# Optimization experiments

Hardware: AMD Instinct MI355X
Metric: run time of the kernel (lower is better)

Reference implementation:

```python
import jax, jax.numpy as jnp
import numpy as np
from jax import lax


def setup_inputs() -> dict:
    key = jax.random.key(0)
    k1, k2 = jax.random.split(key)
    B, H, W, C = 8, 32, 32, 512
    N = 16384
    feature_batch = jax.random.normal(k1, (B, H, W, C), dtype=jnp.float32)
    mb = jax.random.normal(k2, (N, C), dtype=jnp.float32)
    return {"feature_batch": feature_batch, "mb": mb, "b": 9}


def reference(feature_batch, mb, b):
    B, H, W, C = feature_batch.shape
    fv = feature_batch.reshape(B * H * W, C)                       # (Q, C)
    sq = (
        jnp.sum(fv * fv, axis=1)[:, None]
        + jnp.sum(mb * mb, axis=1)[None, :]
        - 2.0 * (fv @ mb.T)
    )                                                               # (Q, N)
    sq = jnp.maximum(sq, 0.0)  # guard fp round-off before sqrt
    # smallest-b distances, sorted ascending (top_k of negated values)
    neg_topk = lax.top_k(-sq, b)[0]                                 # (Q, b)
    top_k_dists_squared = -neg_topk
    pixel_scores = jnp.sqrt(top_k_dists_squared[:, 0]).reshape(B, H * W)
    max_idx = jnp.argmax(pixel_scores, axis=1)                      # (B,)
    softmax_args = jnp.sqrt(
        top_k_dists_squared.reshape(B, H * W, b)[jnp.arange(B), max_idx, :]
    )                                                               # (B, b)
    image_scores = softmax_args[:, 0]
    if b > 1:
        image_scores = image_scores * (1.0 - jax.nn.softmax(softmax_args, axis=1)[:, 0])
    pixel_scores = pixel_scores.reshape(B, 1, H, W)
    return pixel_scores, image_scores
```

## Files before the change

kernel.cpp:

```cpp
#include <hip/hip_runtime.h>

typedef unsigned short u16;

#define M_ROWS 8192
#define N_ROWS 16384
#define KDIM   512
#define BM     256
#define BN     128
#define BK     32
#define NCHUNKS 16
#define NPER   (N_ROWS / NCHUNKS)
#define TOPK   9

#define ASZ (BM * BK)
#define BSZ (BN * BK)
#define NTT ((NPER / BN) * (KDIM / BK))

typedef __attribute__((ext_vector_type(8)))  short bf16x8;
typedef __attribute__((ext_vector_type(16))) float f32x16;

__device__ __forceinline__ void gload_lds16(const void* g, void* l) {
  __builtin_amdgcn_global_load_lds(
      (const __attribute__((address_space(1))) void*)g,
      (__attribute__((address_space(3))) void*)l,
      16, 0, 0);
}

__device__ __forceinline__ u16 f2bf(float x) {
  union { float f; unsigned u; } c; c.f = x;
  unsigned u = c.u;
  u += 0x7fffu + ((u >> 16) & 1u);
  return (u16)(u >> 16);
}

__device__ __forceinline__ void topk_update(float v, float* best) {
  if (v < best[TOPK - 1]) {
    #pragma unroll
    for (int i = 0; i < TOPK; ++i) {
      float b = best[i];
      best[i] = fminf(b, v);
      v = fmaxf(b, v);
    }
  }
}

__global__ __launch_bounds__(256) void prep_kernel(
    const float* __restrict__ fv, const float* __restrict__ mb,
    u16* __restrict__ fvb, u16* __restrict__ mbb,
    float* __restrict__ nf, float* __restrict__ nm_perm)
{
  int idx = blockIdx.x * 4 + (threadIdx.x >> 6);
  int l = threadIdx.x & 63;
  const float* src; u16* dst;
  if (idx < M_ROWS) {
    src = fv + (size_t)idx * KDIM; dst = fvb + (size_t)idx * KDIM;
  } else {
    int r = idx - M_ROWS;
    src = mb + (size_t)r * KDIM; dst = mbb + (size_t)r * KDIM;
  }
  float4 x0 = ((const float4*)src)[2 * l];
  float4 x1 = ((const float4*)src)[2 * l + 1];
  float s = x0.x * x0.x + x0.y * x0.y + x0.z * x0.z + x0.w * x0.w
          + x1.x * x1.x + x1.y * x1.y + x1.z * x1.z + x1.w * x1.w;
  uint4 o;
  o.x = (unsigned)f2bf(x0.x) | ((unsigned)f2bf(x0.y) << 16);
  o.y = (unsigned)f2bf(x0.z) | ((unsigned)f2bf(x0.w) << 16);
  o.z = (unsigned)f2bf(x1.x) | ((unsigned)f2bf(x1.y) << 16);
  o.w = (unsigned)f2bf(x1.z) | ((unsigned)f2bf(x1.w) << 16);
  ((uint4*)dst)[l] = o;
  #pragma unroll
  for (int off = 32; off > 0; off >>= 1) s += __shfl_down(s, off, 64);
  if (l == 0) {
    if (idx < M_ROWS) {
      nf[idx] = s;
    } else {
      int n  = idx - M_ROWS;
      int ig = n >> 5;
      int w5 = n & 31;
      int h  = (w5 >> 2) & 1;
      int r  = (w5 & 3) | ((w5 >> 3) << 2);
      nm_perm[(ig * 2 + h) * 16 + r] = s;
    }
  }
}

__global__ __launch_bounds__(256, 2) void gemm_topk_kernel(
    const u16* __restrict__ fvb, const u16* __restrict__ mbb,
    const float* __restrict__ nm_perm, float* __restrict__ partial)
{
  extern __shared__ __align__(16) u16 sm[];
  u16* const Asm = sm;
  u16* const Bsm = sm + 3 * ASZ;

  const int t   = threadIdx.x;
  const int l   = t & 63;
  const int w   = t >> 6;
  const int h   = l >> 5;
  const int c31 = l & 31;
  const int xr  = (c31 >> 1) & 3;

  const int m0    = blockIdx.x * BM;
  const int ncoff = blockIdx.y * NPER;

  const int srow = l >> 2;
  const int sc   = ((l & 3) ^ ((l >> 3) & 3)) * 8;

  const u16* aSrc = fvb + (size_t)(m0 + w * 64 + srow) * KDIM + sc;
  const u16* bSrc = mbb + (size_t)(ncoff + w * 32 + srow) * KDIM + sc;

  const int aRd  = (w * 64 + c31) * BK;
  const int ch0  = (h ^ xr) * 8;
  const int ch1  = ch0 ^ 16;

#define STAGE(kc2_, bufS_) do {                                               \
    const size_t ao_ = (size_t)((kc2_) & 15) * BK;                            \
    const size_t so_ = (size_t)((kc2_) >> 4) * ((size_t)BN * KDIM) + ao_;     \
    u16* ad_ = Asm + (bufS_) * ASZ + (w * 64) * BK;                           \
    u16* bd_ = Bsm + (bufS_) * BSZ + (w * 32) * BK;                           \
    gload_lds16(aSrc + ao_,                 ad_);                             \
    gload_lds16(aSrc + ao_ + 16 * KDIM,     ad_ + 16 * BK);                   \
    gload_lds16(aSrc + ao_ + 32 * KDIM,     ad_ + 32 * BK);                   \
    gload_lds16(aSrc + ao_ + 48 * KDIM,     ad_ + 48 * BK);                   \
    gload_lds16(bSrc + so_,                 bd_);                             \
    gload_lds16(bSrc + so_ + 16 * KDIM,     bd_ + 16 * BK);                   \
  } while (0)

  float best[2][TOPK];
  float T[2];
  #pragma unroll
  for (int s = 0; s < 2; ++s) {
    T[s] = 3.4e38f;
    #pragma unroll
    for (int i = 0; i < TOPK; ++i) best[s][i] = 3.4e38f;
  }

  f32x16 acc[2][4];

  STAGE(0, 0);
  STAGE(1, 1);
  asm volatile("s_waitcnt vmcnt(6)" ::: "memory");
  __builtin_amdgcn_s_barrier();

  int bC = 0, bS = 2;
  for (int tt = 0; tt < NTT; ++tt) {
    if ((tt & 15) == 0) {
      #pragma unroll
      for (int s = 0; s < 2; ++s)
        #pragma unroll
        for (int i = 0; i < 4; ++i)
          #pragma unroll
          for (int r = 0; r < 16; ++r) acc[s][i][r] = 0.0f;
    }

    const int kc2 = tt + 2;
    if (kc2 < NTT) STAGE(kc2, bS);

    {
      const u16* Ak = Asm + bC * ASZ;
      const u16* Bk = Bsm + bC * BSZ;
      {
        bf16x8 f0 = *(const bf16x8*)&Ak[aRd + ch0];
        bf16x8 f1 = *(const bf16x8*)&Ak[aRd + 32 * BK + ch0];
        #pragma unroll
        for (int i = 0; i < 4; ++i) {
          bf16x8 mbf = *(const bf16x8*)&Bk[(i * 32 + c31) * BK + ch0];
          acc[0][i] = __builtin_amdgcn_mfma_f32_32x32x16_bf16(mbf, f0, acc[0][i], 0, 0, 0);
          acc[1][i] = __builtin_amdgcn_mfma_f32_32x32x16_bf16(mbf, f1, acc[1][i], 0, 0, 0);
        }
      }
      {
        bf16x8 f0 = *(const bf16x8*)&Ak[aRd + ch1];
        bf16x8 f1 = *(const bf16x8*)&Ak[aRd + 32 * BK + ch1];
        #pragma unroll
        for (int i = 0; i < 4; ++i) {
          bf16x8 mbf = *(const bf16x8*)&Bk[(i * 32 + c31) * BK + ch1];
          acc[0][i] = __builtin_amdgcn_mfma_f32_32x32x16_bf16(mbf, f0, acc[0][i], 0, 0, 0);
          acc[1][i] = __builtin_amdgcn_mfma_f32_32x32x16_bf16(mbf, f1, acc[1][i], 0, 0, 0);
        }
      }
    }

    if (tt < NTT - 1) {
      if (tt < NTT - 2) { asm volatile("s_waitcnt vmcnt(6)" ::: "memory"); }
      else              { asm volatile("s_waitcnt vmcnt(0)" ::: "memory"); }
      __builtin_amdgcn_s_barrier();
    }

    if ((tt & 15) == 15) {
      const int nt    = tt >> 4;
      const int nbase = ncoff + nt * BN;
      #pragma unroll
      for (int i = 0; i < 4; ++i) {
        const float4* np = (const float4*)&nm_perm[(((nbase >> 5) + i) * 2 + h) * 16];
        float4 q0 = np[0], q1 = np[1], q2 = np[2], q3 = np[3];
        #pragma unroll
        for (int s = 0; s < 2; ++s) {
          float v[16];
          v[ 0] = fmaf(-2.0f, acc[s][i][ 0], q0.x);
          v[ 1] = fmaf(-2.0f, acc[s][i][ 1], q0.y);
          v[ 2] = fmaf(-2.0f, acc[s][i][ 2], q0.z);
          v[ 3] = fmaf(-2.0f, acc[s][i][ 3], q0.w);
          v[ 4] = fmaf(-2.0f, acc[s][i][ 4], q1.x);
          v[ 5] = fmaf(-2.0f, acc[s][i][ 5], q1.y);
          v[ 6] = fmaf(-2.0f, acc[s][i][ 6], q1.z);
          v[ 7] = fmaf(-2.0f, acc[s][i][ 7], q1.w);
          v[ 8] = fmaf(-2.0f, acc[s][i][ 8], q2.x);
          v[ 9] = fmaf(-2.0f, acc[s][i][ 9], q2.y);
          v[10] = fmaf(-2.0f, acc[s][i][10], q2.z);
          v[11] = fmaf(-2.0f, acc[s][i][11], q2.w);
          v[12] = fmaf(-2.0f, acc[s][i][12], q3.x);
          v[13] = fmaf(-2.0f, acc[s][i][13], q3.y);
          v[14] = fmaf(-2.0f, acc[s][i][14], q3.z);
          v[15] = fmaf(-2.0f, acc[s][i][15], q3.w);
          float bmin = 3.4e38f;
          #pragma unroll
          for (int r = 0; r < 16; ++r) bmin = fminf(bmin, v[r]);
          if (bmin < T[s]) {
            #pragma unroll
            for (int r = 0; r < 16; ++r) topk_update(v[r], best[s]);
            T[s] = best[s][TOPK - 1];
          }
        }
      }
      #pragma unroll
      for (int s = 0; s < 2; ++s)
        T[s] = fminf(best[s][TOPK - 1], __shfl_xor(best[s][TOPK - 1], 32, 64));
    }

    bC = (bC == 2) ? 0 : bC + 1;
    bS = (bS == 2) ? 0 : bS + 1;
  }

  #pragma unroll
  for (int s = 0; s < 2; ++s) {
    float tmp[TOPK];
    #pragma unroll
    for (int q = 0; q < TOPK; ++q) tmp[q] = __shfl_xor(best[s][q], 32, 64);
    #pragma unroll
    for (int q = 0; q < TOPK; ++q) topk_update(tmp[q], best[s]);
    int m = m0 + w * 64 + s * 32 + c31;
    size_t base = ((size_t)blockIdx.y * M_ROWS + m) * TOPK;
    if (h == 0) {
      #pragma unroll
      for (int q = 0; q < 5; ++q) partial[base + q] = best[s][q];
    } else {
      #pragma unroll
      for (int q = 5; q < TOPK; ++q) partial[base + q] = best[s][q];
    }
  }
}

__global__ __launch_bounds__(256) void merge_kernel(
    const float* __restrict__ partial, const float* __restrict__ nf,
    float* __restrict__ final9, float* __restrict__ out_pix)
{
  int row = blockIdx.x * 256 + threadIdx.x;
  float best[TOPK];
  #pragma unroll
  for (int i = 0; i < TOPK; ++i) best[i] = 3.4e38f;
  for (int s = 0; s < NCHUNKS; ++s) {
    const float* p = &partial[((size_t)s * M_ROWS + row) * TOPK];
    #pragma unroll
    for (int i = 0; i < TOPK; ++i) topk_update(p[i], best);
  }
  float nfr = nf[row];
  float d[TOPK];
  #pragma unroll
  for (int i = 0; i < TOPK; ++i) d[i] = sqrtf(fmaxf(best[i] + nfr, 0.0f));
  out_pix[row] = d[0];
  #pragma unroll
  for (int i = 0; i < TOPK; ++i) final9[(size_t)row * TOPK + i] = d[i];
}

__global__ __launch_bounds__(256) void img_kernel(
    const float* __restrict__ out_pix, const float* __restrict__ final9,
    const int* __restrict__ bptr, float* __restrict__ out_img)
{
  int img = blockIdx.x, t = threadIdx.x;
  float bv = -1.0f; int bi = 0;
  for (int p = t; p < 1024; p += 256) {
    float v = out_pix[img * 1024 + p];
    if (v > bv) { bv = v; bi = p; }
  }
  __shared__ float sv[256];
  __shared__ int   si[256];
  sv[t] = bv; si[t] = bi;
  __syncthreads();
  for (int off = 128; off > 0; off >>= 1) {
    if (t < off) {
      float v2 = sv[t + off]; int i2 = si[t + off];
      if (v2 > sv[t] || (v2 == sv[t] && i2 < si[t])) { sv[t] = v2; si[t] = i2; }
    }
    __syncthreads();
  }
  if (t == 0) {
    int row = img * 1024 + si[0];
    int b = bptr[0];
    float s0 = final9[(size_t)row * TOPK + 0];
    float score = s0;
    if (b > 1) {
      int bb = b < TOPK ? b : TOPK;
      float mx = s0;
      for (int i = 1; i < bb; ++i) mx = fmaxf(mx, final9[(size_t)row * TOPK + i]);
      float den = 0.0f;
      for (int i = 0; i < bb; ++i) den += expf(final9[(size_t)row * TOPK + i] - mx);
      score = s0 * (1.0f - expf(s0 - mx) / den);
    }
    out_img[img] = score;
  }
}

extern "C" void kernel_launch(void* const* d_in, const int* in_sizes, int n_in,
                              void* d_out, int out_size, void* d_ws, size_t ws_size,
                              hipStream_t stream) {
  const float* fv   = (const float*)d_in[0];
  const float* mb   = (const float*)d_in[1];
  const int*   bptr = (const int*)d_in[2];
  float* out = (float*)d_out;

  char* ws = (char*)d_ws;
  u16*   fvb     = (u16*)ws;
  u16*   mbb     = (u16*)(ws + 8388608);
  float* nf      = (float*)(ws + 25165824);
  float* nm_perm = (float*)(ws + 25198592);
  float* partial = (float*)(ws + 25264128);
  float* final9  = (float*)(ws + 29982720);

  hipLaunchKernelGGL(prep_kernel, dim3((M_ROWS + N_ROWS) / 4), dim3(256), 0, stream,
                     fv, mb, fvb, mbb, nf, nm_perm);
  hipLaunchKernelGGL(gemm_topk_kernel, dim3(M_ROWS / BM, NCHUNKS), dim3(256),
                     73728, stream, fvb, mbb, nm_perm, partial);
  hipLaunchKernelGGL(merge_kernel, dim3(M_ROWS / 256), dim3(256), 0, stream,
                     partial, nf, final9, out);
  hipLaunchKernelGGL(img_kernel, dim3(8), dim3(256), 0, stream,
                     out, final9, bptr, out + M_ROWS);
}
```

Before: 312.6 us.

## Halve GEMM M-tile and split warps 2x2 with LDS top-k merge

Shrinks the block tile from 256x128 to 128x128 and arranges the four waves as a 2x2 grid over M and N, so each wave computes a 64x64 sub-tile. The grid grows from 32x16 to 64x16 blocks, shared memory per block drops to 48KB and launch bounds allow three blocks per CU, aiming for more parallelism and occupancy. The two N-halves of each row now hold separate top-k lists, which are combined through shared memory before the partial results are written. The cost is lower operand reuse per block (more global and LDS traffic per FLOP) and an extra synchronized merge step.

```diff
diff --git a/kernel.cpp b/kernel.cpp
--- a/kernel.cpp
+++ b/kernel.cpp
@@ -5,7 +5,7 @@
 #define M_ROWS 8192
 #define N_ROWS 16384
 #define KDIM   512
-#define BM     256
+#define BM     128
 #define BN     128
 #define BK     32
 #define NCHUNKS 16
@@ -84,7 +84,7 @@
   }
 }
 
-__global__ __launch_bounds__(256, 2) void gemm_topk_kernel(
+__global__ __launch_bounds__(256, 3) void gemm_topk_kernel(
     const u16* __restrict__ fvb, const u16* __restrict__ mbb,
     const float* __restrict__ nm_perm, float* __restrict__ partial)
 {
@@ -95,6 +95,8 @@
   const int t   = threadIdx.x;
   const int l   = t & 63;
   const int w   = t >> 6;
+  const int wm  = w >> 1;
+  const int wn  = w & 1;
   const int h   = l >> 5;
   const int c31 = l & 31;
   const int xr  = (c31 >> 1) & 3;
@@ -105,24 +107,25 @@
   const int srow = l >> 2;
   const int sc   = ((l & 3) ^ ((l >> 3) & 3)) * 8;
 
-  const u16* aSrc = fvb + (size_t)(m0 + w * 64 + srow) * KDIM + sc;
+  const u16* aSrc = fvb + (size_t)(m0 + w * 32 + srow) * KDIM + sc;
   const u16* bSrc = mbb + (size_t)(ncoff + w * 32 + srow) * KDIM + sc;
 
-  const int aRd  = (w * 64 + c31) * BK;
+  const int aRd0 = (wm * 64 +      c31) * BK;
+  const int aRd1 = (wm * 64 + 32 + c31) * BK;
+  const int bRd0 = (wn * 64 +      c31) * BK;
+  const int bRd1 = (wn * 64 + 32 + c31) * BK;
   const int ch0  = (h ^ xr) * 8;
   const int ch1  = ch0 ^ 16;
 
 #define STAGE(kc2_, bufS_) do {                                               \
     const size_t ao_ = (size_t)((kc2_) & 15) * BK;                            \
     const size_t so_ = (size_t)((kc2_) >> 4) * ((size_t)BN * KDIM) + ao_;     \
-    u16* ad_ = Asm + (bufS_) * ASZ + (w * 64) * BK;                           \
+    u16* ad_ = Asm + (bufS_) * ASZ + (w * 32) * BK;                           \
     u16* bd_ = Bsm + (bufS_) * BSZ + (w * 32) * BK;                           \
-    gload_lds16(aSrc + ao_,                 ad_);                             \
-    gload_lds16(aSrc + ao_ + 16 * KDIM,     ad_ + 16 * BK);                   \
-    gload_lds16(aSrc + ao_ + 32 * KDIM,     ad_ + 32 * BK);                   \
-    gload_lds16(aSrc + ao_ + 48 * KDIM,     ad_ + 48 * BK);                   \
-    gload_lds16(bSrc + so_,                 bd_);                             \
-    gload_lds16(bSrc + so_ + 16 * KDIM,     bd_ + 16 * BK);                   \
+    gload_lds16(aSrc + ao_,             ad_);                                 \
+    gload_lds16(aSrc + ao_ + 16 * KDIM, ad_ + 16 * BK);                       \
+    gload_lds16(bSrc + so_,             bd_);                                 \
+    gload_lds16(bSrc + so_ + 16 * KDIM, bd_ + 16 * BK);                       \
   } while (0)
 
   float best[2][TOPK];
@@ -134,11 +137,11 @@
     for (int i = 0; i < TOPK; ++i) best[s][i] = 3.4e38f;
   }
 
-  f32x16 acc[2][4];
+  f32x16 acc[2][2];
 
   STAGE(0, 0);
   STAGE(1, 1);
-  asm volatile("s_waitcnt vmcnt(6)" ::: "memory");
+  asm volatile("s_waitcnt vmcnt(4)" ::: "memory");
   __builtin_amdgcn_s_barrier();
 
   int bC = 0, bS = 2;
@@ -147,7 +150,7 @@
       #pragma unroll
       for (int s = 0; s < 2; ++s)
         #pragma unroll
-        for (int i = 0; i < 4; ++i)
+        for (int i = 0; i < 2; ++i)
           #pragma unroll
           for (int r = 0; r < 16; ++r) acc[s][i][r] = 0.0f;
     }
@@ -159,29 +162,29 @@
       const u16* Ak = Asm + bC * ASZ;
       const u16* Bk = Bsm + bC * BSZ;
       {
-        bf16x8 f0 = *(const bf16x8*)&Ak[aRd + ch0];
-        bf16x8 f1 = *(const bf16x8*)&Ak[aRd + 32 * BK + ch0];
-        #pragma unroll
-        for (int i = 0; i < 4; ++i) {
-          bf16x8 mbf = *(const bf16x8*)&Bk[(i * 32 + c31) * BK + ch0];
-          acc[0][i] = __builtin_amdgcn_mfma_f32_32x32x16_bf16(mbf, f0, acc[0][i], 0, 0, 0);
-          acc[1][i] = __builtin_amdgcn_mfma_f32_32x32x16_bf16(mbf, f1, acc[1][i], 0, 0, 0);
-        }
+        bf16x8 f0 = *(const bf16x8*)&Ak[aRd0 + ch0];
+        bf16x8 f1 = *(const bf16x8*)&Ak[aRd1 + ch0];
+        bf16x8 g0 = *(const bf16x8*)&Bk[bRd0 + ch0];
+        bf16x8 g1 = *(const bf16x8*)&Bk[bRd1 + ch0];
+        acc[0][0] = __builtin_amdgcn_mfma_f32_32x32x16_bf16(g0, f0, acc[0][0], 0, 0, 0);
+        acc[0][1] = __builtin_amdgcn_mfma_f32_32x32x16_bf16(g1, f0, acc[0][1], 0, 0, 0);
+        acc[1][0] = __builtin_amdgcn_mfma_f32_32x32x16_bf16(g0, f1, acc[1][0], 0, 0, 0);
+        acc[1][1] = __builtin_amdgcn_mfma_f32_32x32x16_bf16(g1, f1, acc[1][1], 0, 0, 0);
       }
       {
-        bf16x8 f0 = *(const bf16x8*)&Ak[aRd + ch1];
-        bf16x8 f1 = *(const bf16x8*)&Ak[aRd + 32 * BK + ch1];
-        #pragma unroll
-        for (int i = 0; i < 4; ++i) {
-          bf16x8 mbf = *(const bf16x8*)&Bk[(i * 32 + c31) * BK + ch1];
-          acc[0][i] = __builtin_amdgcn_mfma_f32_32x32x16_bf16(mbf, f0, acc[0][i], 0, 0, 0);
-          acc[1][i] = __builtin_amdgcn_mfma_f32_32x32x16_bf16(mbf, f1, acc[1][i], 0, 0, 0);
-        }
+        bf16x8 f0 = *(const bf16x8*)&Ak[aRd0 + ch1];
+        bf16x8 f1 = *(const bf16x8*)&Ak[aRd1 + ch1];
+        bf16x8 g0 = *(const bf16x8*)&Bk[bRd0 + ch1];
+        bf16x8 g1 = *(const bf16x8*)&Bk[bRd1 + ch1];
+        acc[0][0] = __builtin_amdgcn_mfma_f32_32x32x16_bf16(g0, f0, acc[0][0], 0, 0, 0);
+        acc[0][1] = __builtin_amdgcn_mfma_f32_32x32x16_bf16(g1, f0, acc[0][1], 0, 0, 0);
+        acc[1][0] = __builtin_amdgcn_mfma_f32_32x32x16_bf16(g0, f1, acc[1][0], 0, 0, 0);
+        acc[1][1] = __builtin_amdgcn_mfma_f32_32x32x16_bf16(g1, f1, acc[1][1], 0, 0, 0);
       }
     }
 
     if (tt < NTT - 1) {
-      if (tt < NTT - 2) { asm volatile("s_waitcnt vmcnt(6)" ::: "memory"); }
+      if (tt < NTT - 2) { asm volatile("s_waitcnt vmcnt(4)" ::: "memory"); }
       else              { asm volatile("s_waitcnt vmcnt(0)" ::: "memory"); }
       __builtin_amdgcn_s_barrier();
     }
@@ -190,8 +193,9 @@
       const int nt    = tt >> 4;
       const int nbase = ncoff + nt * BN;
       #pragma unroll
-      for (int i = 0; i < 4; ++i) {
-        const float4* np = (const float4*)&nm_perm[(((nbase >> 5) + i) * 2 + h) * 16];
+      for (int i = 0; i < 2; ++i) {
+        const float4* np =
+            (const float4*)&nm_perm[(((nbase >> 5) + wn * 2 + i) * 2 + h) * 16];
         float4 q0 = np[0], q1 = np[1], q2 = np[2], q3 = np[3];
         #pragma unroll
         for (int s = 0; s < 2; ++s) {
@@ -238,14 +242,33 @@
     for (int q = 0; q < TOPK; ++q) tmp[q] = __shfl_xor(best[s][q], 32, 64);
     #pragma unroll
     for (int q = 0; q < TOPK; ++q) topk_update(tmp[q], best[s]);
-    int m = m0 + w * 64 + s * 32 + c31;
-    size_t base = ((size_t)blockIdx.y * M_ROWS + m) * TOPK;
-    if (h == 0) {
-      #pragma unroll
-      for (int q = 0; q < 5; ++q) partial[base + q] = best[s][q];
-    } else {
-      #pragma unroll
-      for (int q = 5; q < TOPK; ++q) partial[base + q] = best[s][q];
+  }
+
+  float* smerge = (float*)sm;
+  __syncthreads();
+  if (wn == 1 && h == 0) {
+    #pragma unroll
+    for (int s = 0; s < 2; ++s)
+      #pragma unroll
+      for (int q = 0; q < TOPK; ++q)
+        smerge[(wm * 64 + s * 32 + c31) * TOPK + q] = best[s][q];
+  }
+  __syncthreads();
+  if (wn == 0) {
+    #pragma unroll
+    for (int s = 0; s < 2; ++s) {
+      const float* p = &smerge[(wm * 64 + s * 32 + c31) * TOPK];
+      #pragma unroll
+      for (int q = 0; q < TOPK; ++q) topk_update(p[q], best[s]);
+      int m = m0 + wm * 64 + s * 32 + c31;
+      size_t base = ((size_t)blockIdx.y * M_ROWS + m) * TOPK;
+      if (h == 0) {
+        #pragma unroll
+        for (int q = 0; q < 5; ++q) partial[base + q] = best[s][q];
+      } else {
+        #pragma unroll
+        for (int q = 5; q < TOPK; ++q) partial[base + q] = best[s][q];
+      }
     }
   }
 }
@@ -329,7 +352,7 @@
   hipLaunchKernelGGL(prep_kernel, dim3((M_ROWS + N_ROWS) / 4), dim3(256), 0, stream,
                      fv, mb, fvb, mbb, nf, nm_perm);
   hipLaunchKernelGGL(gemm_topk_kernel, dim3(M_ROWS / BM, NCHUNKS), dim3(256),
-                     73728, stream, fvb, mbb, nm_perm, partial);
+                     49152, stream, fvb, mbb, nm_perm, partial);
   hipLaunchKernelGGL(merge_kernel, dim3(M_ROWS / 256), dim3(256), 0, stream,
                      partial, nf, final9, out);
   hipLaunchKernelGGL(img_kernel, dim3(8), dim3(256), 0, stream,
```

Result: slower. 348.3 us (+11.4%).

## Fold memory-bank norms into GEMM via extended K and fuse merge with image scoring

Applied to the files above, without the earlier changes.

Extends K from 512 to 544 and packs -||m||^2/2 as a bf16 hi/lo pair against constant 1.0 entries in the query rows, so the MFMA accumulator directly holds x·m - ||m||^2/2. The epilogue then runs a top-k on maxima without loading the permuted norm array or doing per-element FMAs, and scales by -2 only at the final write. The merge and image kernels are fused into one 8-block kernel that recomputes the top-9 for the argmax row, removing the final9 buffer and one launch. The extra K slice adds about 6% more MFMA work and global loads, the merge now runs on only 8 blocks, and the bf16 split of the norm brings a small precision risk.

```diff
diff --git a/kernel.cpp b/kernel.cpp
--- a/kernel.cpp
+++ b/kernel.cpp
@@ -5,6 +5,7 @@
 #define M_ROWS 8192
 #define N_ROWS 16384
 #define KDIM   512
+#define KEXT   544
 #define BM     256
 #define BN     128
 #define BK     32
@@ -14,7 +15,8 @@
 
 #define ASZ (BM * BK)
 #define BSZ (BN * BK)
-#define NTT ((NPER / BN) * (KDIM / BK))
+#define KT  (KEXT / BK)
+#define NTT ((NPER / BN) * KT)
 
 typedef __attribute__((ext_vector_type(8)))  short bf16x8;
 typedef __attribute__((ext_vector_type(16))) float f32x16;
@@ -33,6 +35,11 @@
   return (u16)(u >> 16);
 }
 
+__device__ __forceinline__ float bf2f(u16 x) {
+  union { unsigned u; float f; } c; c.u = ((unsigned)x) << 16;
+  return c.f;
+}
+
 __device__ __forceinline__ void topk_update(float v, float* best) {
   if (v < best[TOPK - 1]) {
     #pragma unroll
@@ -44,19 +51,30 @@
   }
 }
 
+__device__ __forceinline__ void topk_update_max(float v, float* best) {
+  if (v > best[TOPK - 1]) {
+    #pragma unroll
+    for (int i = 0; i < TOPK; ++i) {
+      float b = best[i];
+      best[i] = fmaxf(b, v);
+      v = fminf(b, v);
+    }
+  }
+}
+
 __global__ __launch_bounds__(256) void prep_kernel(
     const float* __restrict__ fv, const float* __restrict__ mb,
-    u16* __restrict__ fvb, u16* __restrict__ mbb,
-    float* __restrict__ nf, float* __restrict__ nm_perm)
+    u16* __restrict__ fvb, u16* __restrict__ mbb, float* __restrict__ nf)
 {
   int idx = blockIdx.x * 4 + (threadIdx.x >> 6);
   int l = threadIdx.x & 63;
   const float* src; u16* dst;
-  if (idx < M_ROWS) {
-    src = fv + (size_t)idx * KDIM; dst = fvb + (size_t)idx * KDIM;
+  const bool isf = idx < M_ROWS;
+  if (isf) {
+    src = fv + (size_t)idx * KDIM; dst = fvb + (size_t)idx * KEXT;
   } else {
     int r = idx - M_ROWS;
-    src = mb + (size_t)r * KDIM; dst = mbb + (size_t)r * KDIM;
+    src = mb + (size_t)r * KDIM; dst = mbb + (size_t)r * KEXT;
   }
   float4 x0 = ((const float4*)src)[2 * l];
   float4 x1 = ((const float4*)src)[2 * l + 1];
@@ -69,24 +87,29 @@
   o.w = (unsigned)f2bf(x1.z) | ((unsigned)f2bf(x1.w) << 16);
   ((uint4*)dst)[l] = o;
   #pragma unroll
-  for (int off = 32; off > 0; off >>= 1) s += __shfl_down(s, off, 64);
-  if (l == 0) {
-    if (idx < M_ROWS) {
-      nf[idx] = s;
-    } else {
-      int n  = idx - M_ROWS;
-      int ig = n >> 5;
-      int w5 = n & 31;
-      int h  = (w5 >> 2) & 1;
-      int r  = (w5 & 3) | ((w5 >> 3) << 2);
-      nm_perm[(ig * 2 + h) * 16 + r] = s;
-    }
-  }
+  for (int off = 32; off > 0; off >>= 1) s += __shfl_xor(s, off, 64);
+  if (l < 4) {
+    uint4 z = {0u, 0u, 0u, 0u};
+    if (l == 0) {
+      unsigned e01;
+      if (isf) {
+        e01 = 0x3F80u | (0x3F80u << 16);
+      } else {
+        float a = 0.5f * s;
+        u16 ah = f2bf(a);
+        u16 al = f2bf(a - bf2f(ah));
+        e01 = (unsigned)(ah ^ 0x8000u) | ((unsigned)(al ^ 0x8000u) << 16);
+      }
+      z.x = e01;
+    }
+    ((uint4*)(dst + KDIM))[l] = z;
+  }
+  if (isf && l == 0) nf[idx] = s;
 }
 
 __global__ __launch_bounds__(256, 2) void gemm_topk_kernel(
     const u16* __restrict__ fvb, const u16* __restrict__ mbb,
-    const float* __restrict__ nm_perm, float* __restrict__ partial)
+    float* __restrict__ partial)
 {
   extern __shared__ __align__(16) u16 sm[];
   u16* const Asm = sm;
@@ -105,45 +128,49 @@
   const int srow = l >> 2;
   const int sc   = ((l & 3) ^ ((l >> 3) & 3)) * 8;
 
-  const u16* aSrc = fvb + (size_t)(m0 + w * 64 + srow) * KDIM + sc;
-  const u16* bSrc = mbb + (size_t)(ncoff + w * 32 + srow) * KDIM + sc;
+  const u16* aSrc = fvb + (size_t)(m0 + w * 64 + srow) * KEXT + sc;
+  const u16* bSrc = mbb + (size_t)(ncoff + w * 32 + srow) * KEXT + sc;
 
   const int aRd  = (w * 64 + c31) * BK;
+  const int bRd  = c31 * BK;
   const int ch0  = (h ^ xr) * 8;
   const int ch1  = ch0 ^ 16;
 
-#define STAGE(kc2_, bufS_) do {                                               \
-    const size_t ao_ = (size_t)((kc2_) & 15) * BK;                            \
-    const size_t so_ = (size_t)((kc2_) >> 4) * ((size_t)BN * KDIM) + ao_;     \
+#define STAGE(koS_, nOffS_, bufS_) do {                                       \
+    const u16* as_ = aSrc + (koS_) * BK;                                      \
+    const u16* bs_ = bSrc + (nOffS_) + (koS_) * BK;                           \
     u16* ad_ = Asm + (bufS_) * ASZ + (w * 64) * BK;                           \
     u16* bd_ = Bsm + (bufS_) * BSZ + (w * 32) * BK;                           \
-    gload_lds16(aSrc + ao_,                 ad_);                             \
-    gload_lds16(aSrc + ao_ + 16 * KDIM,     ad_ + 16 * BK);                   \
-    gload_lds16(aSrc + ao_ + 32 * KDIM,     ad_ + 32 * BK);                   \
-    gload_lds16(aSrc + ao_ + 48 * KDIM,     ad_ + 48 * BK);                   \
-    gload_lds16(bSrc + so_,                 bd_);                             \
-    gload_lds16(bSrc + so_ + 16 * KDIM,     bd_ + 16 * BK);                   \
+    gload_lds16(as_,             ad_);                                        \
+    gload_lds16(as_ + 16 * KEXT, ad_ + 16 * BK);                              \
+    gload_lds16(as_ + 32 * KEXT, ad_ + 32 * BK);                              \
+    gload_lds16(as_ + 48 * KEXT, ad_ + 48 * BK);                              \
+    gload_lds16(bs_,             bd_);                                        \
+    gload_lds16(bs_ + 16 * KEXT, bd_ + 16 * BK);                              \
   } while (0)
 
   float best[2][TOPK];
   float T[2];
   #pragma unroll
   for (int s = 0; s < 2; ++s) {
-    T[s] = 3.4e38f;
-    #pragma unroll
-    for (int i = 0; i < TOPK; ++i) best[s][i] = 3.4e38f;
+    T[s] = -3.4e38f;
+    #pragma unroll
+    for (int i = 0; i < TOPK; ++i) best[s][i] = -3.4e38f;
   }
 
   f32x16 acc[2][4];
 
-  STAGE(0, 0);
-  STAGE(1, 1);
+  STAGE(0, 0, 0);
+  STAGE(1, 0, 1);
   asm volatile("s_waitcnt vmcnt(6)" ::: "memory");
   __builtin_amdgcn_s_barrier();
 
   int bC = 0, bS = 2;
+  int ko = 0;
+  int ko2 = 2;
+  int nOff2 = 0;
   for (int tt = 0; tt < NTT; ++tt) {
-    if ((tt & 15) == 0) {
+    if (ko == 0) {
       #pragma unroll
       for (int s = 0; s < 2; ++s)
         #pragma unroll
@@ -152,28 +179,27 @@
           for (int r = 0; r < 16; ++r) acc[s][i][r] = 0.0f;
     }
 
-    const int kc2 = tt + 2;
-    if (kc2 < NTT) STAGE(kc2, bS);
+    if (tt + 2 < NTT) STAGE(ko2, nOff2, bS);
 
     {
       const u16* Ak = Asm + bC * ASZ;
       const u16* Bk = Bsm + bC * BSZ;
       {
         bf16x8 f0 = *(const bf16x8*)&Ak[aRd + ch0];
-        bf16x8 f1 = *(const bf16x8*)&Ak[aRd + 32 * BK + ch0];
+        bf16x8 f1 = *(const bf16x8*)&Ak[aRd + 1024 + ch0];
         #pragma unroll
         for (int i = 0; i < 4; ++i) {
-          bf16x8 mbf = *(const bf16x8*)&Bk[(i * 32 + c31) * BK + ch0];
+          bf16x8 mbf = *(const bf16x8*)&Bk[bRd + i * 1024 + ch0];
           acc[0][i] = __builtin_amdgcn_mfma_f32_32x32x16_bf16(mbf, f0, acc[0][i], 0, 0, 0);
           acc[1][i] = __builtin_amdgcn_mfma_f32_32x32x16_bf16(mbf, f1, acc[1][i], 0, 0, 0);
         }
       }
       {
         bf16x8 f0 = *(const bf16x8*)&Ak[aRd + ch1];
-        bf16x8 f1 = *(const bf16x8*)&Ak[aRd + 32 * BK + ch1];
+        bf16x8 f1 = *(const bf16x8*)&Ak[aRd + 1024 + ch1];
         #pragma unroll
         for (int i = 0; i < 4; ++i) {
-          bf16x8 mbf = *(const bf16x8*)&Bk[(i * 32 + c31) * BK + ch1];
+          bf16x8 mbf = *(const bf16x8*)&Bk[bRd + i * 1024 + ch1];
           acc[0][i] = __builtin_amdgcn_mfma_f32_32x32x16_bf16(mbf, f0, acc[0][i], 0, 0, 0);
           acc[1][i] = __builtin_amdgcn_mfma_f32_32x32x16_bf16(mbf, f1, acc[1][i], 0, 0, 0);
         }
@@ -186,49 +212,30 @@
       __builtin_amdgcn_s_barrier();
     }
 
-    if ((tt & 15) == 15) {
-      const int nt    = tt >> 4;
-      const int nbase = ncoff + nt * BN;
+    if (ko == 16) {
       #pragma unroll
       for (int i = 0; i < 4; ++i) {
-        const float4* np = (const float4*)&nm_perm[(((nbase >> 5) + i) * 2 + h) * 16];
-        float4 q0 = np[0], q1 = np[1], q2 = np[2], q3 = np[3];
         #pragma unroll
         for (int s = 0; s < 2; ++s) {
-          float v[16];
-          v[ 0] = fmaf(-2.0f, acc[s][i][ 0], q0.x);
-          v[ 1] = fmaf(-2.0f, acc[s][i][ 1], q0.y);
-          v[ 2] = fmaf(-2.0f, acc[s][i][ 2], q0.z);
-          v[ 3] = fmaf(-2.0f, acc[s][i][ 3], q0.w);
-          v[ 4] = fmaf(-2.0f, acc[s][i][ 4], q1.x);
-          v[ 5] = fmaf(-2.0f, acc[s][i][ 5], q1.y);
-          v[ 6] = fmaf(-2.0f, acc[s][i][ 6], q1.z);
-          v[ 7] = fmaf(-2.0f, acc[s][i][ 7], q1.w);
-          v[ 8] = fmaf(-2.0f, acc[s][i][ 8], q2.x);
-          v[ 9] = fmaf(-2.0f, acc[s][i][ 9], q2.y);
-          v[10] = fmaf(-2.0f, acc[s][i][10], q2.z);
-          v[11] = fmaf(-2.0f, acc[s][i][11], q2.w);
-          v[12] = fmaf(-2.0f, acc[s][i][12], q3.x);
-          v[13] = fmaf(-2.0f, acc[s][i][13], q3.y);
-          v[14] = fmaf(-2.0f, acc[s][i][14], q3.z);
-          v[15] = fmaf(-2.0f, acc[s][i][15], q3.w);
-          float bmin = 3.4e38f;
+          float bmax = acc[s][i][0];
           #pragma unroll
-          for (int r = 0; r < 16; ++r) bmin = fminf(bmin, v[r]);
-          if (bmin < T[s]) {
+          for (int r = 1; r < 16; ++r) bmax = fmaxf(bmax, acc[s][i][r]);
+          if (bmax > T[s]) {
             #pragma unroll
-            for (int r = 0; r < 16; ++r) topk_update(v[r], best[s]);
+            for (int r = 0; r < 16; ++r) topk_update_max(acc[s][i][r], best[s]);
             T[s] = best[s][TOPK - 1];
           }
         }
       }
       #pragma unroll
       for (int s = 0; s < 2; ++s)
-        T[s] = fminf(best[s][TOPK - 1], __shfl_xor(best[s][TOPK - 1], 32, 64));
+        T[s] = fmaxf(best[s][TOPK - 1], __shfl_xor(best[s][TOPK - 1], 32, 64));
     }
 
     bC = (bC == 2) ? 0 : bC + 1;
     bS = (bS == 2) ? 0 : bS + 1;
+    ko = (ko == 16) ? 0 : ko + 1;
+    if (ko2 == 16) { ko2 = 0; nOff2 += BN * KEXT; } else { ++ko2; }
   }
 
   #pragma unroll
@@ -237,53 +244,43 @@
     #pragma unroll
     for (int q = 0; q < TOPK; ++q) tmp[q] = __shfl_xor(best[s][q], 32, 64);
     #pragma unroll
-    for (int q = 0; q < TOPK; ++q) topk_update(tmp[q], best[s]);
+    for (int q = 0; q < TOPK; ++q) topk_update_max(tmp[q], best[s]);
     int m = m0 + w * 64 + s * 32 + c31;
     size_t base = ((size_t)blockIdx.y * M_ROWS + m) * TOPK;
     if (h == 0) {
       #pragma unroll
-      for (int q = 0; q < 5; ++q) partial[base + q] = best[s][q];
+      for (int q = 0; q < 5; ++q) partial[base + q] = -2.0f * best[s][q];
     } else {
       #pragma unroll
-      for (int q = 5; q < TOPK; ++q) partial[base + q] = best[s][q];
-    }
-  }
-}
-
-__global__ __launch_bounds__(256) void merge_kernel(
+      for (int q = 5; q < TOPK; ++q) partial[base + q] = -2.0f * best[s][q];
+    }
+  }
+}
+
+__global__ __launch_bounds__(256) void merge_img_kernel(
     const float* __restrict__ partial, const float* __restrict__ nf,
-    float* __restrict__ final9, float* __restrict__ out_pix)
+    const int* __restrict__ bptr, float* __restrict__ out_pix,
+    float* __restrict__ out_img)
 {
-  int row = blockIdx.x * 256 + threadIdx.x;
-  float best[TOPK];
-  #pragma unroll
-  for (int i = 0; i < TOPK; ++i) best[i] = 3.4e38f;
-  for (int s = 0; s < NCHUNKS; ++s) {
-    const float* p = &partial[((size_t)s * M_ROWS + row) * TOPK];
-    #pragma unroll
-    for (int i = 0; i < TOPK; ++i) topk_update(p[i], best);
-  }
-  float nfr = nf[row];
-  float d[TOPK];
-  #pragma unroll
-  for (int i = 0; i < TOPK; ++i) d[i] = sqrtf(fmaxf(best[i] + nfr, 0.0f));
-  out_pix[row] = d[0];
-  #pragma unroll
-  for (int i = 0; i < TOPK; ++i) final9[(size_t)row * TOPK + i] = d[i];
-}
-
-__global__ __launch_bounds__(256) void img_kernel(
-    const float* __restrict__ out_pix, const float* __restrict__ final9,
-    const int* __restrict__ bptr, float* __restrict__ out_img)
-{
-  int img = blockIdx.x, t = threadIdx.x;
-  float bv = -1.0f; int bi = 0;
-  for (int p = t; p < 1024; p += 256) {
-    float v = out_pix[img * 1024 + p];
-    if (v > bv) { bv = v; bi = p; }
-  }
+  const int img = blockIdx.x, t = threadIdx.x;
   __shared__ float sv[256];
   __shared__ int   si[256];
+  float bv = -1.0f; int bi = 0;
+  for (int k = 0; k < 4; ++k) {
+    int p = t + k * 256;
+    int row = img * 1024 + p;
+    float best[TOPK];
+    #pragma unroll
+    for (int i = 0; i < TOPK; ++i) best[i] = 3.4e38f;
+    for (int s = 0; s < NCHUNKS; ++s) {
+      const float* pp = &partial[((size_t)s * M_ROWS + row) * TOPK];
+      #pragma unroll
+      for (int i = 0; i < TOPK; ++i) topk_update(pp[i], best);
+    }
+    float d0 = sqrtf(fmaxf(best[0] + nf[row], 0.0f));
+    out_pix[row] = d0;
+    if (d0 > bv) { bv = d0; bi = p; }
+  }
   sv[t] = bv; si[t] = bi;
   __syncthreads();
   for (int off = 128; off > 0; off >>= 1) {
@@ -295,15 +292,27 @@
   }
   if (t == 0) {
     int row = img * 1024 + si[0];
+    float best[TOPK];
+    #pragma unroll
+    for (int i = 0; i < TOPK; ++i) best[i] = 3.4e38f;
+    for (int s = 0; s < NCHUNKS; ++s) {
+      const float* pp = &partial[((size_t)s * M_ROWS + row) * TOPK];
+      #pragma unroll
+      for (int i = 0; i < TOPK; ++i) topk_update(pp[i], best);
+    }
+    float nfr = nf[row];
+    float d[TOPK];
+    #pragma unroll
+    for (int i = 0; i < TOPK; ++i) d[i] = sqrtf(fmaxf(best[i] + nfr, 0.0f));
     int b = bptr[0];
-    float s0 = final9[(size_t)row * TOPK + 0];
+    float s0 = d[0];
     float score = s0;
     if (b > 1) {
       int bb = b < TOPK ? b : TOPK;
       float mx = s0;
-      for (int i = 1; i < bb; ++i) mx = fmaxf(mx, final9[(size_t)row * TOPK + i]);
+      for (int i = 1; i < bb; ++i) mx = fmaxf(mx, d[i]);
       float den = 0.0f;
-      for (int i = 0; i < bb; ++i) den += expf(final9[(size_t)row * TOPK + i] - mx);
+      for (int i = 0; i < bb; ++i) den += expf(d[i] - mx);
       score = s0 * (1.0f - expf(s0 - mx) / den);
     }
     out_img[img] = score;
@@ -320,18 +329,14 @@
 
   char* ws = (char*)d_ws;
   u16*   fvb     = (u16*)ws;
-  u16*   mbb     = (u16*)(ws + 8388608);
-  float* nf      = (float*)(ws + 25165824);
-  float* nm_perm = (float*)(ws + 25198592);
-  float* partial = (float*)(ws + 25264128);
-  float* final9  = (float*)(ws + 29982720);
+  u16*   mbb     = (u16*)(ws + 8912896);
+  float* nf      = (float*)(ws + 26738688);
+  float* partial = (float*)(ws + 26771456);
 
   hipLaunchKernelGGL(prep_kernel, dim3((M_ROWS + N_ROWS) / 4), dim3(256), 0, stream,
-                     fv, mb, fvb, mbb, nf, nm_perm);
+                     fv, mb, fvb, mbb, nf);
   hipLaunchKernelGGL(gemm_topk_kernel, dim3(M_ROWS / BM, NCHUNKS), dim3(256),
-                     73728, stream, fvb, mbb, nm_perm, partial);
-  hipLaunchKernelGGL(merge_kernel, dim3(M_ROWS / 256), dim3(256), 0, stream,
-                     partial, nf, final9, out);
-  hipLaunchKernelGGL(img_kernel, dim3(8), dim3(256), 0, stream,
-                     out, final9, bptr, out + M_ROWS);
-}
+                     73728, stream, fvb, mbb, partial);
+  hipLaunchKernelGGL(merge_img_kernel, dim3(8), dim3(256), 0, stream,
+                     partial, nf, bptr, out, out + M_ROWS);
+}
```

Measured after the change: 397.1 us. 1.27x slower.

## Widen GEMM tile to 256x256 with 8 waves and in-LDS top-k merge

Applied to the files above, without the earlier changes.

Doubles the N tile (BN 128->256) and the block to 512 threads arranged as a 4x2 wave grid, so each block reuses its A tile across twice as many memory-bank columns. Each wave now stages only 2 A and 2 B rows per k-step, and the waitcnt values are adjusted to match. The two N-half waves holding the same rows merge their top-9 lists through LDS before writing partial results. This costs more LDS per block (96KB), which may limit occupancy, and adds an extra merge step with barriers.

```diff
diff --git a/kernel.cpp b/kernel.cpp
--- a/kernel.cpp
+++ b/kernel.cpp
@@ -6,7 +6,7 @@
 #define N_ROWS 16384
 #define KDIM   512
 #define BM     256
-#define BN     128
+#define BN     256
 #define BK     32
 #define NCHUNKS 16
 #define NPER   (N_ROWS / NCHUNKS)
@@ -84,7 +84,7 @@
   }
 }
 
-__global__ __launch_bounds__(256, 2) void gemm_topk_kernel(
+__global__ __launch_bounds__(512, 2) void gemm_topk_kernel(
     const u16* __restrict__ fvb, const u16* __restrict__ mbb,
     const float* __restrict__ nm_perm, float* __restrict__ partial)
 {
@@ -95,6 +95,8 @@
   const int t   = threadIdx.x;
   const int l   = t & 63;
   const int w   = t >> 6;
+  const int wm  = w >> 1;
+  const int wn  = w & 1;
   const int h   = l >> 5;
   const int c31 = l & 31;
   const int xr  = (c31 >> 1) & 3;
@@ -105,24 +107,23 @@
   const int srow = l >> 2;
   const int sc   = ((l & 3) ^ ((l >> 3) & 3)) * 8;
 
-  const u16* aSrc = fvb + (size_t)(m0 + w * 64 + srow) * KDIM + sc;
+  const u16* aSrc = fvb + (size_t)(m0 + w * 32 + srow) * KDIM + sc;
   const u16* bSrc = mbb + (size_t)(ncoff + w * 32 + srow) * KDIM + sc;
 
-  const int aRd  = (w * 64 + c31) * BK;
+  const int aRd  = (wm * 64 + c31) * BK;
+  const int bRd  = (wn * 128 + c31) * BK;
   const int ch0  = (h ^ xr) * 8;
   const int ch1  = ch0 ^ 16;
 
-#define STAGE(kc2_, bufS_) do {                                               \
-    const size_t ao_ = (size_t)((kc2_) & 15) * BK;                            \
-    const size_t so_ = (size_t)((kc2_) >> 4) * ((size_t)BN * KDIM) + ao_;     \
-    u16* ad_ = Asm + (bufS_) * ASZ + (w * 64) * BK;                           \
+#define STAGE(tt2_, bufS_) do {                                               \
+    const size_t ao_ = (size_t)((tt2_) & 15) * BK;                            \
+    const size_t bo_ = (size_t)((tt2_) >> 4) * ((size_t)BN * KDIM) + ao_;     \
+    u16* ad_ = Asm + (bufS_) * ASZ + (w * 32) * BK;                           \
     u16* bd_ = Bsm + (bufS_) * BSZ + (w * 32) * BK;                           \
-    gload_lds16(aSrc + ao_,                 ad_);                             \
-    gload_lds16(aSrc + ao_ + 16 * KDIM,     ad_ + 16 * BK);                   \
-    gload_lds16(aSrc + ao_ + 32 * KDIM,     ad_ + 32 * BK);                   \
-    gload_lds16(aSrc + ao_ + 48 * KDIM,     ad_ + 48 * BK);                   \
-    gload_lds16(bSrc + so_,                 bd_);                             \
-    gload_lds16(bSrc + so_ + 16 * KDIM,     bd_ + 16 * BK);                   \
+    gload_lds16(aSrc + ao_,             ad_);                                 \
+    gload_lds16(aSrc + ao_ + 16 * KDIM, ad_ + 16 * BK);                       \
+    gload_lds16(bSrc + bo_,             bd_);                                 \
+    gload_lds16(bSrc + bo_ + 16 * KDIM, bd_ + 16 * BK);                       \
   } while (0)
 
   float best[2][TOPK];
@@ -138,7 +139,7 @@
 
   STAGE(0, 0);
   STAGE(1, 1);
-  asm volatile("s_waitcnt vmcnt(6)" ::: "memory");
+  asm volatile("s_waitcnt vmcnt(4)" ::: "memory");
   __builtin_amdgcn_s_barrier();
 
   int bC = 0, bS = 2;
@@ -152,8 +153,7 @@
           for (int r = 0; r < 16; ++r) acc[s][i][r] = 0.0f;
     }
 
-    const int kc2 = tt + 2;
-    if (kc2 < NTT) STAGE(kc2, bS);
+    if (tt + 2 < NTT) STAGE(tt + 2, bS);
 
     {
       const u16* Ak = Asm + bC * ASZ;
@@ -163,7 +163,7 @@
         bf16x8 f1 = *(const bf16x8*)&Ak[aRd + 32 * BK + ch0];
         #pragma unroll
         for (int i = 0; i < 4; ++i) {
-          bf16x8 mbf = *(const bf16x8*)&Bk[(i * 32 + c31) * BK + ch0];
+          bf16x8 mbf = *(const bf16x8*)&Bk[bRd + i * 32 * BK + ch0];
           acc[0][i] = __builtin_amdgcn_mfma_f32_32x32x16_bf16(mbf, f0, acc[0][i], 0, 0, 0);
           acc[1][i] = __builtin_amdgcn_mfma_f32_32x32x16_bf16(mbf, f1, acc[1][i], 0, 0, 0);
         }
@@ -173,7 +173,7 @@
         bf16x8 f1 = *(const bf16x8*)&Ak[aRd + 32 * BK + ch1];
         #pragma unroll
         for (int i = 0; i < 4; ++i) {
-          bf16x8 mbf = *(const bf16x8*)&Bk[(i * 32 + c31) * BK + ch1];
+          bf16x8 mbf = *(const bf16x8*)&Bk[bRd + i * 32 * BK + ch1];
           acc[0][i] = __builtin_amdgcn_mfma_f32_32x32x16_bf16(mbf, f0, acc[0][i], 0, 0, 0);
           acc[1][i] = __builtin_amdgcn_mfma_f32_32x32x16_bf16(mbf, f1, acc[1][i], 0, 0, 0);
         }
@@ -181,7 +181,7 @@
     }
 
     if (tt < NTT - 1) {
-      if (tt < NTT - 2) { asm volatile("s_waitcnt vmcnt(6)" ::: "memory"); }
+      if (tt < NTT - 2) { asm volatile("s_waitcnt vmcnt(4)" ::: "memory"); }
       else              { asm volatile("s_waitcnt vmcnt(0)" ::: "memory"); }
       __builtin_amdgcn_s_barrier();
     }
@@ -191,7 +191,8 @@
       const int nbase = ncoff + nt * BN;
       #pragma unroll
       for (int i = 0; i < 4; ++i) {
-        const float4* np = (const float4*)&nm_perm[(((nbase >> 5) + i) * 2 + h) * 16];
+        const float4* np =
+            (const float4*)&nm_perm[(((nbase >> 5) + wn * 4 + i) * 2 + h) * 16];
         float4 q0 = np[0], q1 = np[1], q2 = np[2], q3 = np[3];
         #pragma unroll
         for (int s = 0; s < 2; ++s) {
@@ -238,14 +239,33 @@
     for (int q = 0; q < TOPK; ++q) tmp[q] = __shfl_xor(best[s][q], 32, 64);
     #pragma unroll
     for (int q = 0; q < TOPK; ++q) topk_update(tmp[q], best[s]);
-    int m = m0 + w * 64 + s * 32 + c31;
-    size_t base = ((size_t)blockIdx.y * M_ROWS + m) * TOPK;
-    if (h == 0) {
-      #pragma unroll
-      for (int q = 0; q < 5; ++q) partial[base + q] = best[s][q];
-    } else {
-      #pragma unroll
-      for (int q = 5; q < TOPK; ++q) partial[base + q] = best[s][q];
+  }
+
+  float* smerge = (float*)sm;
+  __syncthreads();
+  if (wn == 1 && h == 0) {
+    #pragma unroll
+    for (int s = 0; s < 2; ++s)
+      #pragma unroll
+      for (int q = 0; q < TOPK; ++q)
+        smerge[(wm * 64 + s * 32 + c31) * TOPK + q] = best[s][q];
+  }
+  __syncthreads();
+  if (wn == 0) {
+    #pragma unroll
+    for (int s = 0; s < 2; ++s) {
+      const float* p = &smerge[(wm * 64 + s * 32 + c31) * TOPK];
+      #pragma unroll
+      for (int q = 0; q < TOPK; ++q) topk_update(p[q], best[s]);
+      int m = m0 + wm * 64 + s * 32 + c31;
+      size_t base = ((size_t)blockIdx.y * M_ROWS + m) * TOPK;
+      if (h == 0) {
+        #pragma unroll
+        for (int q = 0; q < 5; ++q) partial[base + q] = best[s][q];
+      } else {
+        #pragma unroll
+        for (int q = 5; q < TOPK; ++q) partial[base + q] = best[s][q];
+      }
     }
   }
 }
@@ -328,8 +348,8 @@
 
   hipLaunchKernelGGL(prep_kernel, dim3((M_ROWS + N_ROWS) / 4), dim3(256), 0, stream,
                      fv, mb, fvb, mbb, nf, nm_perm);
-  hipLaunchKernelGGL(gemm_topk_kernel, dim3(M_ROWS / BM, NCHUNKS), dim3(256),
-                     73728, stream, fvb, mbb, nm_perm, partial);
+  hipLaunchKernelGGL(gemm_topk_kernel, dim3(M_ROWS / BM, NCHUNKS), dim3(512),
+                     98304, stream, fvb, mbb, nm_perm, partial);
   hipLaunchKernelGGL(merge_kernel, dim3(M_ROWS / 256), dim3(256), 0, stream,
                      partial, nf, final9, out);
   hipLaunchKernelGGL(img_kernel, dim3(8), dim3(256), 0, stream,
```

Measured after the change: 344.7 us. 1.1x slower.
